# Optimization experiments

Measured on AMD Instinct MI355X. Metric: run time of the kernel, lower is better.

Reference implementation:

```python
import jax, jax.numpy as jnp
import numpy as np

N_INST = 100000
N_NET = 100000
E = 1600000
H = 64
OUT = 32
L = 2


def setup_inputs() -> dict:
    key = jax.random.key(0)
    ks = jax.random.split(key, 16)
    inp = {
        "x_inst": jax.random.normal(ks[0], (N_INST, H), jnp.float32),
        "x_net": jax.random.normal(ks[1], (N_NET, H), jnp.float32),
        "edge_i2n": jax.random.randint(ks[2], (2, E), 0, N_INST, jnp.int32),
        "edge_n2i": jax.random.randint(ks[3], (2, E), 0, N_NET, jnp.int32),
        # stacked GAT params: axis0 = layer, axis1 = relation (0: inst->net, 1: net->inst)
        "W_src": jax.random.normal(ks[4], (L, 2, H, H), jnp.float32) * 0.1,
        "W_dst": jax.random.normal(ks[5], (L, 2, H, H), jnp.float32) * 0.1,
        "att_src": jax.random.normal(ks[6], (L, 2, H), jnp.float32) * 0.1,
        "att_dst": jax.random.normal(ks[7], (L, 2, H), jnp.float32) * 0.1,
        "bias_g": jax.random.normal(ks[8], (L, 2, H), jnp.float32) * 0.1,
        "lin1_w": jax.random.normal(ks[9], (H, OUT), jnp.float32) * 0.1,
        "lin1_b": jax.random.normal(ks[10], (OUT,), jnp.float32) * 0.1,
        "lin2_w": jax.random.normal(ks[11], (OUT, 1), jnp.float32) * 0.1,
        "lin2_b": jax.random.normal(ks[12], (1,), jnp.float32) * 0.1,
    }
    return inp


def _segment_softmax(scores, seg, n_seg):
    # numerically stable softmax over edges grouped by destination node
    m = jax.ops.segment_max(scores, seg, num_segments=n_seg)
    e = jnp.exp(scores - m[seg])
    s = jax.ops.segment_sum(e, seg, num_segments=n_seg)
    return e / (s[seg] + 1e-16)


def _gat_conv(x_src, x_dst, edge, Ws, Wd, a_s, a_d, b, n_dst):
    # PyG GATConv, heads=1, add_self_loops=False, eval mode (dropout inactive)
    hs = x_src @ Ws  # [Ns, H]
    hd = x_dst @ Wd  # [Nd, H]
    src, dst = edge[0], edge[1]
    score = (hs * a_s).sum(-1)[src] + (hd * a_d).sum(-1)[dst]  # [E]
    alpha = _segment_softmax(jax.nn.leaky_relu(score, 0.2), dst, n_dst)
    out = jax.ops.segment_sum(hs[src] * alpha[:, None], dst, num_segments=n_dst)
    return out + b


def reference(x_inst, x_net, edge_i2n, edge_n2i, W_src, W_dst, att_src, att_dst,
              bias_g, lin1_w, lin1_b, lin2_w, lin2_b):
    xi, xn = x_inst, x_net
    for l in range(L):
        new_net = _gat_conv(xi, xn, edge_i2n, W_src[l, 0], W_dst[l, 0],
                            att_src[l, 0], att_dst[l, 0], bias_g[l, 0], xn.shape[0])
        new_inst = _gat_conv(xn, xi, edge_n2i, W_src[l, 1], W_dst[l, 1],
                             att_src[l, 1], att_dst[l, 1], bias_g[l, 1], xi.shape[0])
        xn = jax.nn.relu(new_net)
        xi = jax.nn.relu(new_inst)
    h = jax.nn.relu(xn @ lin1_w + lin1_b)
    return h @ lin2_w + lin2_b  # [N_net, 1]
```

## Files before the change

kernel.cpp:

```cpp
#include <hip/hip_runtime.h>
#include <hip/hip_fp16.h>

#define H 64
#define BSHIFT 9
#define BUCKET 512
#define NBMAX 256
#define CHUNK 4096

__device__ __forceinline__ int bcasti(int x, int j) {
    return __builtin_amdgcn_readlane(x, j);
}
__device__ __forceinline__ float bcastf(float x, int j) {
    return __uint_as_float((unsigned)__builtin_amdgcn_readlane((int)__float_as_uint(x), j));
}

__device__ __forceinline__ float ldf(const float* p) { return *p; }
__device__ __forceinline__ float ldf(const __half* p) { return __half2float(*p); }

__global__ void wvec3_kernel(const float* __restrict__ W_dst, const float* __restrict__ att_dst,
                             float* __restrict__ v2all) {
    int b = blockIdx.x;
    int k = threadIdx.x;
    const float* Wd = W_dst + (size_t)b * H * H;
    const float* ad = att_dst + (size_t)b * H;
    float s2 = 0.f;
    for (int j = 0; j < H; ++j) s2 += Wd[k * H + j] * ad[j];
    v2all[b * H + k] = s2;
}

template <typename T>
__device__ __forceinline__ void proj_body(float* __restrict__ Wl, int blk,
                                          const T* __restrict__ x, const float* __restrict__ W,
                                          const float* __restrict__ as_, const float* __restrict__ v2d,
                                          __half* __restrict__ hs, float* __restrict__ ssrc,
                                          float* __restrict__ sdst_out, int n) {
    int t = threadIdx.x;
    for (int i = t; i < H * H; i += 256) Wl[i] = W[i];
    __syncthreads();
    int lane = t & 63;
    int w = t >> 6;
    int row0 = blk * 16 + w * 4;
    if (row0 >= n) return;
    int rem = n - row0;
    float asl = as_[lane];
    const T* xp = x + (size_t)row0 * H + lane;
    float xr0 = ldf(xp);
    float xr1 = rem > 1 ? ldf(xp + H) : 0.f;
    float xr2 = rem > 2 ? ldf(xp + 2 * H) : 0.f;
    float xr3 = rem > 3 ? ldf(xp + 3 * H) : 0.f;
    float a0 = 0.f, a1 = 0.f, a2 = 0.f, a3 = 0.f;
#pragma unroll
    for (int k = 0; k < H; ++k) {
        float wv = Wl[k * H + lane];
        a0 = fmaf(bcastf(xr0, k), wv, a0);
        a1 = fmaf(bcastf(xr1, k), wv, a1);
        a2 = fmaf(bcastf(xr2, k), wv, a2);
        a3 = fmaf(bcastf(xr3, k), wv, a3);
    }
    __half* hp = hs + (size_t)row0 * H + lane;
    hp[0] = __float2half_rn(a0);
    if (rem > 1) hp[H] = __float2half_rn(a1);
    if (rem > 2) hp[2 * H] = __float2half_rn(a2);
    if (rem > 3) hp[3 * H] = __float2half_rn(a3);
    float p0 = a0 * asl, p1 = a1 * asl, p2 = a2 * asl, p3 = a3 * asl;
#pragma unroll
    for (int off = 32; off; off >>= 1) {
        p0 += __shfl_xor(p0, off); p1 += __shfl_xor(p1, off);
        p2 += __shfl_xor(p2, off); p3 += __shfl_xor(p3, off);
    }
    if (lane == 0) {
        ssrc[row0] = p0;
        if (rem > 1) ssrc[row0 + 1] = p1;
        if (rem > 2) ssrc[row0 + 2] = p2;
        if (rem > 3) ssrc[row0 + 3] = p3;
    }
    if (sdst_out) {
        float vl = v2d[lane];
        float q0 = xr0 * vl, q1 = xr1 * vl, q2 = xr2 * vl, q3 = xr3 * vl;
#pragma unroll
        for (int off = 32; off; off >>= 1) {
            q0 += __shfl_xor(q0, off); q1 += __shfl_xor(q1, off);
            q2 += __shfl_xor(q2, off); q3 += __shfl_xor(q3, off);
        }
        if (lane == 0) {
            sdst_out[row0] = q0;
            if (rem > 1) sdst_out[row0 + 1] = q1;
            if (rem > 2) sdst_out[row0 + 2] = q2;
            if (rem > 3) sdst_out[row0 + 3] = q3;
        }
    }
}

__global__ void hist_proj_kernel(const int* __restrict__ dstA, const int* __restrict__ dstB,
                                 int* __restrict__ cntA, int* __restrict__ cntB,
                                 int ne, int nch, int nbA, int nbB,
                                 const float* __restrict__ x, const float* __restrict__ W,
                                 const float* __restrict__ as_, const float* __restrict__ v2d,
                                 __half* __restrict__ hs, float* __restrict__ ssrc,
                                 float* __restrict__ sdst_out, int n) {
    __shared__ float smem[H * H];
    int blk = blockIdx.x;
    if (blk < 2 * nch) {
        int* h = (int*)smem;
        bool second = blk >= nch;
        const int* dst = second ? dstB : dstA;
        int* cnt = second ? cntB : cntA;
        int nb = second ? nbB : nbA;
        int c = second ? blk - nch : blk;
        int beg = c * CHUNK, end = beg + CHUNK;
        if (end > ne) end = ne;
        int t = threadIdx.x;
        for (int i = t; i < NBMAX; i += 256) h[i] = 0;
        __syncthreads();
        for (int i = beg + t; i < end; i += 256) atomicAdd(&h[dst[i] >> BSHIFT], 1);
        __syncthreads();
        for (int b = t; b < nb; b += 256) cnt[(size_t)b * nch + c] = h[b];
        return;
    }
    proj_body<float>(smem, blk - 2 * nch, x, W, as_, v2d, hs, ssrc, sdst_out, n);
}

__global__ void scan_chunks(int* __restrict__ cntA, int* __restrict__ cntB,
                            int* __restrict__ totA, int* __restrict__ totB,
                            int nch, int nbA) {
    __shared__ int sm[512];
    int b = blockIdx.x;
    bool second = b >= nbA;
    int* cnt = second ? cntB : cntA;
    int* tot = second ? totB : totA;
    if (second) b -= nbA;
    int t = threadIdx.x;
    int v = t < nch ? cnt[(size_t)b * nch + t] : 0;
    sm[t] = v;
    __syncthreads();
    for (int off = 1; off < 512; off <<= 1) {
        int u = t >= off ? sm[t - off] : 0;
        __syncthreads();
        sm[t] += u;
        __syncthreads();
    }
    if (t < nch) cnt[(size_t)b * nch + t] = sm[t] - v;
    if (t == 511) tot[b] = sm[511];
}

__global__ void scan_buckets(const int* __restrict__ totA, const int* __restrict__ totB,
                             int* __restrict__ bstartA, int* __restrict__ bstartB,
                             int nbA, int nbB, int ne) {
    __shared__ int sm[256];
    const int* tot = blockIdx.x ? totB : totA;
    int* bstart = blockIdx.x ? bstartB : bstartA;
    int nb = blockIdx.x ? nbB : nbA;
    int t = threadIdx.x;
    int v = t < nb ? tot[t] : 0;
    sm[t] = v;
    __syncthreads();
    for (int off = 1; off < 256; off <<= 1) {
        int u = t >= off ? sm[t - off] : 0;
        __syncthreads();
        sm[t] += u;
        __syncthreads();
    }
    if (t < nb) bstart[t] = sm[t] - v;
    if (t == 0) bstart[nb] = ne;
}

__global__ void scatter_proj_kernel(const int* __restrict__ srcA, const int* __restrict__ dstA,
                                    const int* __restrict__ cntA, const int* __restrict__ bstartA,
                                    unsigned* __restrict__ tmpA,
                                    const int* __restrict__ srcB, const int* __restrict__ dstB,
                                    const int* __restrict__ cntB, const int* __restrict__ bstartB,
                                    unsigned* __restrict__ tmpB,
                                    int ne, int nch, int nbA, int nbB,
                                    const float* __restrict__ x, const float* __restrict__ W,
                                    const float* __restrict__ as_, const float* __restrict__ v2d,
                                    __half* __restrict__ hs, float* __restrict__ ssrc,
                                    float* __restrict__ sdst_out, int n) {
    __shared__ float smem[H * H];
    int blk = blockIdx.x;
    if (blk < 2 * nch) {
        int* cur = (int*)smem;
        bool second = blk >= nch;
        const int* src = second ? srcB : srcA;
        const int* dst = second ? dstB : dstA;
        const int* cnt = second ? cntB : cntA;
        const int* bstart = second ? bstartB : bstartA;
        unsigned* tmp = second ? tmpB : tmpA;
        int nb = second ? nbB : nbA;
        int c = second ? blk - nch : blk;
        int beg = c * CHUNK, end = beg + CHUNK;
        if (end > ne) end = ne;
        int t = threadIdx.x;
        for (int b = t; b < nb; b += 256) cur[b] = bstart[b] + cnt[(size_t)b * nch + c];
        __syncthreads();
        for (int i = beg + t; i < end; i += 256) {
            int d = dst[i];
            int pos = atomicAdd(&cur[d >> BSHIFT], 1);
            unsigned rec = ((unsigned)(d & (BUCKET - 1)) << 17) | (unsigned)src[i];
            tmp[pos] = rec;
        }
        return;
    }
    proj_body<float>(smem, blk - 2 * nch, x, W, as_, v2d, hs, ssrc, sdst_out, n);
}

__global__ void proj_half_kernel(const __half* __restrict__ x, const float* __restrict__ W,
                                 const float* __restrict__ as_,
                                 __half* __restrict__ hs, float* __restrict__ ssrc, int n) {
    __shared__ float smem[H * H];
    proj_body<__half>(smem, blockIdx.x, x, W, as_, nullptr, hs, ssrc, nullptr, n);
}

__global__ void bucket_finalize(const unsigned* __restrict__ tmpA, const int* __restrict__ bstartA,
                                int* __restrict__ rowptrA, int* __restrict__ srcsA,
                                int ndstA, int nbA,
                                const unsigned* __restrict__ tmpB, const int* __restrict__ bstartB,
                                int* __restrict__ rowptrB, int* __restrict__ srcsB,
                                int ndstB) {
    __shared__ int cnt[BUCKET];
    __shared__ int sm[BUCKET];
    __shared__ int cur[BUCKET];
    int b = blockIdx.x;
    bool second = b >= nbA;
    const unsigned* tmp = second ? tmpB : tmpA;
    const int* bstart = second ? bstartB : bstartA;
    int* rowptr = second ? rowptrB : rowptrA;
    int* srcs   = second ? srcsB : srcsA;
    int ndst    = second ? ndstB : ndstA;
    if (second) b -= nbA;

    int t = threadIdx.x;
    int base = bstart[b], endi = bstart[b + 1];
    cnt[t] = 0;
    __syncthreads();
    for (int i = base + t; i < endi; i += 512)
        atomicAdd(&cnt[tmp[i] >> 17], 1);
    __syncthreads();
    int c0 = cnt[t];
    sm[t] = c0;
    __syncthreads();
    for (int off = 1; off < 512; off <<= 1) {
        int u = t >= off ? sm[t - off] : 0;
        __syncthreads();
        sm[t] += u;
        __syncthreads();
    }
    int d0 = b << BSHIFT;
    int e = base + sm[t] - c0;
    cur[t] = e;
    if (d0 + t < ndst) rowptr[d0 + t] = e;
    if (t == 0) {
        int hi = d0 + BUCKET;
        if (hi > ndst) hi = ndst;
        rowptr[hi] = endi;
    }
    __syncthreads();
    for (int i = base + t; i < endi; i += 512) {
        unsigned rec = tmp[i];
        int pos = atomicAdd(&cur[rec >> 17], 1);
        srcs[pos] = (int)(rec & 0x1FFFFu);
    }
}

template <int P>
__device__ __forceinline__ float gat_fast(const int* __restrict__ srcs, int beg, int cnt,
                                          const float* __restrict__ ssrc, float sdst,
                                          const __half* __restrict__ hs,
                                          const float* __restrict__ bias, int lane) {
    bool valid = lane < cnt;
    int s_l = valid ? srcs[beg + lane] : 0;
    float ss = valid ? ssrc[s_l] : 0.f;

    const __half* hsl = hs + lane;
    __half hv[P];
#pragma unroll
    for (int k = 0; k < P; ++k) {
        hv[k] = hsl[(size_t)bcasti(s_l, k) * H];
    }

    float sc = ss + sdst;
    sc = sc > 0.f ? sc : 0.2f * sc;
    float ev_l = valid ? __expf(sc) : 0.f;
    float ll = ev_l;
#pragma unroll
    for (int off = 32; off; off >>= 1) ll += __shfl_xor(ll, off);

    float acc0 = 0.f, acc1 = 0.f, acc2 = 0.f, acc3 = 0.f;
    float acc4 = 0.f, acc5 = 0.f, acc6 = 0.f, acc7 = 0.f;
#pragma unroll
    for (int k = 0; k < P; k += 8) {
        acc0 += bcastf(ev_l, k + 0) * __half2float(hv[k + 0]);
        acc1 += bcastf(ev_l, k + 1) * __half2float(hv[k + 1]);
        acc2 += bcastf(ev_l, k + 2) * __half2float(hv[k + 2]);
        acc3 += bcastf(ev_l, k + 3) * __half2float(hv[k + 3]);
        acc4 += bcastf(ev_l, k + 4) * __half2float(hv[k + 4]);
        acc5 += bcastf(ev_l, k + 5) * __half2float(hv[k + 5]);
        acc6 += bcastf(ev_l, k + 6) * __half2float(hv[k + 6]);
        acc7 += bcastf(ev_l, k + 7) * __half2float(hv[k + 7]);
    }
    if constexpr (P == 32) {
        int j = P;
        for (; j + 3 < cnt; j += 4) {
            acc0 += bcastf(ev_l, j + 0) * __half2float(hsl[(size_t)bcasti(s_l, j + 0) * H]);
            acc1 += bcastf(ev_l, j + 1) * __half2float(hsl[(size_t)bcasti(s_l, j + 1) * H]);
            acc2 += bcastf(ev_l, j + 2) * __half2float(hsl[(size_t)bcasti(s_l, j + 2) * H]);
            acc3 += bcastf(ev_l, j + 3) * __half2float(hsl[(size_t)bcasti(s_l, j + 3) * H]);
        }
        for (; j < cnt; ++j)
            acc0 += bcastf(ev_l, j) * __half2float(hsl[(size_t)bcasti(s_l, j) * H]);
    }
    float v = ((acc0 + acc1) + (acc2 + acc3)) + ((acc4 + acc5) + (acc6 + acc7));
    v = v / (ll + 1e-16f) + bias[lane];
    return v > 0.f ? v : 0.f;
}

__device__ __forceinline__ float gat_general(const int* __restrict__ srcs, int beg, int end,
                                             const float* __restrict__ ssrc, float sdst,
                                             const __half* __restrict__ hs,
                                             const float* __restrict__ bias, int lane) {
    const __half* hsl = hs + lane;
    float acc0 = 0.f, acc1 = 0.f;
    float mm = -3.4e38f;
    for (int base = beg; base < end; base += 64) {
        int idx = base + lane;
        if (idx < end) {
            float sc = ssrc[srcs[idx]] + sdst;
            sc = sc > 0.f ? sc : 0.2f * sc;
            mm = fmaxf(mm, sc);
        }
    }
#pragma unroll
    for (int off = 32; off; off >>= 1) mm = fmaxf(mm, __shfl_xor(mm, off));
    float ll = 0.f;
    for (int base = beg; base < end; base += 64) {
        int idx = base + lane;
        int c2 = end - base; if (c2 > 64) c2 = 64;
        int s_l = idx < end ? srcs[idx] : 0;
        float ev_l = 0.f;
        if (idx < end) {
            float sc = ssrc[s_l] + sdst;
            sc = sc > 0.f ? sc : 0.2f * sc;
            ev_l = __expf(sc - mm);
        }
        ll += ev_l;
        int j = 0;
        for (; j + 1 < c2; j += 2) {
            acc0 += bcastf(ev_l, j) * __half2float(hsl[(size_t)bcasti(s_l, j) * H]);
            acc1 += bcastf(ev_l, j + 1) * __half2float(hsl[(size_t)bcasti(s_l, j + 1) * H]);
        }
        if (j < c2)
            acc0 += bcastf(ev_l, j) * __half2float(hsl[(size_t)bcasti(s_l, j) * H]);
    }
#pragma unroll
    for (int off = 32; off; off >>= 1) ll += __shfl_xor(ll, off);
    float v = (acc0 + acc1) / (ll + 1e-16f) + bias[lane];
    return v > 0.f ? v : 0.f;
}

__device__ __forceinline__ float gat_aggregate(const int* __restrict__ rowptr,
                                               const int* __restrict__ srcs,
                                               const float* __restrict__ ssrc,
                                               float sdst,
                                               const __half* __restrict__ hs,
                                               const float* __restrict__ bias,
                                               int wid, int lane) {
    int beg = rowptr[wid], end = rowptr[wid + 1];
    int cnt = end - beg;
    if (cnt <= 16) return gat_fast<16>(srcs, beg, cnt, ssrc, sdst, hs, bias, lane);
    if (cnt <= 64) return gat_fast<32>(srcs, beg, cnt, ssrc, sdst, hs, bias, lane);
    return gat_general(srcs, beg, end, ssrc, sdst, hs, bias, lane);
}

template <int P>
__device__ __forceinline__ float2 gat_pair_fast(const int* __restrict__ srcs,
                                                int r0, int r1, int cnt0, int cnt1,
                                                const float* __restrict__ ssrc,
                                                float sdstA, float sdstB,
                                                const __half* __restrict__ hs,
                                                const float* __restrict__ bias,
                                                int lane) {
    int half = lane >> 5, sub = lane & 31;
    int beg = half ? r1 : r0;
    int cnt = half ? cnt1 : cnt0;
    bool valid = sub < cnt;
    int s_l = valid ? srcs[beg + sub] : 0;
    float ss = valid ? ssrc[s_l] : 0.f;
    float sdst = half ? sdstB : sdstA;

    const __half2* hp = (const __half2*)hs;
    __half2 hv[P];
#pragma unroll
    for (int k = 0; k < P; ++k) {
        int sA = bcasti(s_l, k), sB = bcasti(s_l, 32 + k);
        int srow = half ? sB : sA;
        hv[k] = hp[(size_t)srow * 32 + sub];
    }

    float sc = ss + sdst;
    sc = sc > 0.f ? sc : 0.2f * sc;
    float ev_l = valid ? __expf(sc) : 0.f;
    float ll = ev_l;
#pragma unroll
    for (int off = 16; off; off >>= 1) ll += __shfl_xor(ll, off);

    float ax0 = 0.f, ax1 = 0.f, ax2 = 0.f, ax3 = 0.f;
    float ay0 = 0.f, ay1 = 0.f, ay2 = 0.f, ay3 = 0.f;
#pragma unroll
    for (int k = 0; k < P; k += 4) {
#pragma unroll
        for (int u = 0; u < 4; ++u) {
            float eA = bcastf(ev_l, k + u), eB = bcastf(ev_l, 32 + k + u);
            float e = half ? eB : eA;
            float2 f = __half22float2(hv[k + u]);
            if (u == 0) { ax0 += e * f.x; ay0 += e * f.y; }
            if (u == 1) { ax1 += e * f.x; ay1 += e * f.y; }
            if (u == 2) { ax2 += e * f.x; ay2 += e * f.y; }
            if (u == 3) { ax3 += e * f.x; ay3 += e * f.y; }
        }
    }
    float vx = (ax0 + ax1) + (ax2 + ax3);
    float vy = (ay0 + ay1) + (ay2 + ay3);
    float inv = 1.f / (ll + 1e-16f);
    float2 bv = *(const float2*)(bias + 2 * sub);
    vx = vx * inv + bv.x;
    vy = vy * inv + bv.y;
    vx = vx > 0.f ? vx : 0.f;
    vy = vy > 0.f ? vy : 0.f;
    return make_float2(vx, vy);
}

__global__ void gat1_kernel(const int* __restrict__ rp, const int* __restrict__ sr,
                            const float* __restrict__ ssrc, const float* __restrict__ sdstArr,
                            const __half* __restrict__ hs, const float* __restrict__ bias,
                            __half* __restrict__ out, int n) {
    int t = (int)(blockIdx.x * blockDim.x + threadIdx.x);
    int pw = t >> 6, lane = t & 63;
    int wid0 = 2 * pw;
    if (wid0 >= n) return;
    bool has1 = wid0 + 1 < n;
    int r0 = rp[wid0], r1 = rp[wid0 + 1];
    int r2 = has1 ? rp[wid0 + 2] : r1;
    int cnt0 = r1 - r0, cnt1 = r2 - r1;
    int mx = cnt0 > cnt1 ? cnt0 : cnt1;
    int half = lane >> 5, sub = lane & 31;

    if (mx <= 32) {
        float sdstA = sdstArr[wid0];
        float sdstB = has1 ? sdstArr[wid0 + 1] : 0.f;
        float2 v;
        if (mx <= 16) v = gat_pair_fast<16>(sr, r0, r1, cnt0, cnt1, ssrc, sdstA, sdstB, hs, bias, lane);
        else          v = gat_pair_fast<32>(sr, r0, r1, cnt0, cnt1, ssrc, sdstA, sdstB, hs, bias, lane);
        int node = half ? wid0 + 1 : wid0;
        if (!half || has1)
            *(__half2*)(out + (size_t)node * H + 2 * sub) = __float22half2_rn(v);
    } else {
        float v0 = gat_aggregate(rp, sr, ssrc, sdstArr[wid0], hs, bias, wid0, lane);
        out[(size_t)wid0 * H + lane] = __float2half_rn(v0);
        if (has1) {
            float v1 = gat_aggregate(rp, sr, ssrc, sdstArr[wid0 + 1], hs, bias, wid0 + 1, lane);
            out[(size_t)(wid0 + 1) * H + lane] = __float2half_rn(v1);
        }
    }
}

template <int P>
__device__ __forceinline__ float gat02_fast(const int* __restrict__ srcs, int beg, int cnt,
                                            const float* __restrict__ ssrc0, float sdst0,
                                            const __half* __restrict__ hs0, const float* __restrict__ bias0,
                                            const float* __restrict__ v2next,
                                            const float* __restrict__ ssrc2,
                                            const __half* __restrict__ hs2, const float* __restrict__ bias2,
                                            int lane) {
    bool valid = lane < cnt;
    int s_l = valid ? srcs[beg + lane] : 0;
    float ss0 = valid ? ssrc0[s_l] : 0.f;
    float ss2 = valid ? ssrc2[s_l] : 0.f;

    const __half* h0 = hs0 + lane;
    const __half* h2 = hs2 + lane;
    __half hv0[P], hv2[P];
#pragma unroll
    for (int k = 0; k < P; ++k) hv0[k] = h0[(size_t)bcasti(s_l, k) * H];
#pragma unroll
    for (int k = 0; k < P; ++k) hv2[k] = h2[(size_t)bcasti(s_l, k) * H];

    float sc0 = ss0 + sdst0;
    sc0 = sc0 > 0.f ? sc0 : 0.2f * sc0;
    float ev0 = valid ? __expf(sc0) : 0.f;
    float l0 = ev0;
#pragma unroll
    for (int off = 32; off; off >>= 1) l0 += __shfl_xor(l0, off);

    float a0 = 0.f, a1 = 0.f, a2 = 0.f, a3 = 0.f;
#pragma unroll
    for (int k = 0; k < P; k += 4) {
        a0 += bcastf(ev0, k + 0) * __half2float(hv0[k + 0]);
        a1 += bcastf(ev0, k + 1) * __half2float(hv0[k + 1]);
        a2 += bcastf(ev0, k + 2) * __half2float(hv0[k + 2]);
        a3 += bcastf(ev0, k + 3) * __half2float(hv0[k + 3]);
    }
    if constexpr (P == 32) {
        int j = P;
        for (; j < cnt; ++j)
            a0 += bcastf(ev0, j) * __half2float(h0[(size_t)bcasti(s_l, j) * H]);
    }
    float v0 = ((a0 + a1) + (a2 + a3)) / (l0 + 1e-16f) + bias0[lane];
    v0 = v0 > 0.f ? v0 : 0.f;

    float q = v0 * v2next[lane];
#pragma unroll
    for (int off = 32; off; off >>= 1) q += __shfl_xor(q, off);

    float sc2 = ss2 + q;
    sc2 = sc2 > 0.f ? sc2 : 0.2f * sc2;
    float ev2 = valid ? __expf(sc2) : 0.f;
    float l2 = ev2;
#pragma unroll
    for (int off = 32; off; off >>= 1) l2 += __shfl_xor(l2, off);

    float b0 = 0.f, b1 = 0.f, b2_ = 0.f, b3 = 0.f;
#pragma unroll
    for (int k = 0; k < P; k += 4) {
        b0 += bcastf(ev2, k + 0) * __half2float(hv2[k + 0]);
        b1 += bcastf(ev2, k + 1) * __half2float(hv2[k + 1]);
        b2_ += bcastf(ev2, k + 2) * __half2float(hv2[k + 2]);
        b3 += bcastf(ev2, k + 3) * __half2float(hv2[k + 3]);
    }
    if constexpr (P == 32) {
        int j = P;
        for (; j < cnt; ++j)
            b0 += bcastf(ev2, j) * __half2float(h2[(size_t)bcasti(s_l, j) * H]);
    }
    float v2 = ((b0 + b1) + (b2_ + b3)) / (l2 + 1e-16f) + bias2[lane];
    return v2 > 0.f ? v2 : 0.f;
}

__global__ void gat02_mlp_kernel(const int* __restrict__ rowptr, const int* __restrict__ srcs,
                                 const float* __restrict__ ssrc0, const float* __restrict__ sdst0Arr,
                                 const __half* __restrict__ hs0, const float* __restrict__ bias0,
                                 const float* __restrict__ v2next,
                                 const float* __restrict__ ssrc2, const __half* __restrict__ hs2,
                                 const float* __restrict__ bias2,
                                 const float* __restrict__ w1, const float* __restrict__ b1,
                                 const float* __restrict__ w2, const float* __restrict__ b2,
                                 float* __restrict__ out, int ndst) {
    __shared__ float W1[H * 32];
    __shared__ float W2[32];
    __shared__ float B1[32];
    {
        int t = threadIdx.x;
        for (int i = t; i < H * 32; i += 256) W1[i] = w1[i];
        if (t < 32) { W2[t] = w2[t]; B1[t] = b1[t]; }
        __syncthreads();
    }
    int wid = (int)((blockIdx.x * blockDim.x + threadIdx.x) >> 6);
    int lane = threadIdx.x & 63;
    if (wid >= ndst) return;

    int beg = rowptr[wid], end = rowptr[wid + 1];
    int cnt = end - beg;
    float v;
    if (cnt <= 16) {
        v = gat02_fast<16>(srcs, beg, cnt, ssrc0, sdst0Arr[wid], hs0, bias0,
                           v2next, ssrc2, hs2, bias2, lane);
    } else if (cnt <= 64) {
        v = gat02_fast<32>(srcs, beg, cnt, ssrc0, sdst0Arr[wid], hs0, bias0,
                           v2next, ssrc2, hs2, bias2, lane);
    } else {
        float v0 = gat_general(srcs, beg, end, ssrc0, sdst0Arr[wid], hs0, bias0, lane);
        float q = v0 * v2next[lane];
#pragma unroll
        for (int off = 32; off; off >>= 1) q += __shfl_xor(q, off);
        v = gat_general(srcs, beg, end, ssrc2, q, hs2, bias2, lane);
    }

    int c = lane & 31;
    int kbase = (lane >> 5) << 5;
    float s = 0.f;
#pragma unroll
    for (int k = 0; k < 32; ++k) s += __shfl(v, kbase + k) * W1[(kbase + k) * 32 + c];
    s += __shfl_xor(s, 32);
    s += B1[c];
    s = s > 0.f ? s : 0.f;
    float q = s * W2[c];
#pragma unroll
    for (int off = 16; off; off >>= 1) q += __shfl_xor(q, off);
    if (lane == 0) out[wid] = q + b2[0];
}

extern "C" void kernel_launch(void* const* d_in, const int* in_sizes, int n_in,
                              void* d_out, int out_size, void* d_ws, size_t ws_size,
                              hipStream_t stream) {
    const float* x_inst  = (const float*)d_in[0];
    const float* x_net   = (const float*)d_in[1];
    const int*   e_i2n   = (const int*)d_in[2];
    const int*   e_n2i   = (const int*)d_in[3];
    const float* W_src   = (const float*)d_in[4];
    const float* W_dst   = (const float*)d_in[5];
    const float* att_src = (const float*)d_in[6];
    const float* att_dst = (const float*)d_in[7];
    const float* bias_g  = (const float*)d_in[8];
    const float* lin1_w  = (const float*)d_in[9];
    const float* lin1_b  = (const float*)d_in[10];
    const float* lin2_w  = (const float*)d_in[11];
    const float* lin2_b  = (const float*)d_in[12];

    const int n_inst = in_sizes[0] / H;
    const int n_net  = in_sizes[1] / H;
    const int ne     = in_sizes[2] / 2;
    const int nmax   = n_inst > n_net ? n_inst : n_net;

    const int nbA = (n_net + BUCKET - 1) >> BSHIFT;
    const int nbB = (n_inst + BUCKET - 1) >> BSHIFT;
    const int nch = (ne + CHUNK - 1) / CHUNK;

    float* ws = (float*)d_ws;
    size_t off = 0;
    auto alloc = [&](size_t nelem) {
        off = (off + 3) & ~(size_t)3;
        float* p = ws + off; off += nelem; return p;
    };
    __half* xiA    = (__half*)alloc((size_t)n_inst * H / 2);
    __half* hs0    = (__half*)alloc((size_t)nmax * H / 2);
    __half* hs1    = (__half*)alloc((size_t)nmax * H / 2);
    __half* hs2    = (__half*)alloc((size_t)nmax * H / 2);
    float* ssrc0   = alloc(nmax);
    float* ssrc1   = alloc(nmax);
    float* ssrc2   = alloc(nmax);
    float* sdstA   = alloc(nmax);
    float* sdstB   = alloc(nmax);
    int*   rp_i2n  = (int*)alloc(nmax + 1);
    int*   sr_i2n  = (int*)alloc(ne);
    int*   rp_n2i  = (int*)alloc(nmax + 1);
    int*   sr_n2i  = (int*)alloc(ne);
    unsigned* tmpA = (unsigned*)alloc(ne);
    unsigned* tmpB = (unsigned*)alloc(ne);
    int*   cntA    = (int*)alloc((size_t)NBMAX * nch);
    int*   cntB    = (int*)alloc((size_t)NBMAX * nch);
    int*   totA    = (int*)alloc(NBMAX);
    int*   totB    = (int*)alloc(NBMAX);
    int*   bstartA = (int*)alloc(NBMAX + 1);
    int*   bstartB = (int*)alloc(NBMAX + 1);
    float* v2all   = alloc(3 * H);
    (void)ws_size;

    const int* dstA = e_i2n + ne;
    const int* dstB = e_n2i + ne;

    wvec3_kernel<<<3, 64, 0, stream>>>(W_dst, att_dst, v2all);

    {
        int grid = 2 * nch + (n_inst + 15) / 16;
        hist_proj_kernel<<<grid, 256, 0, stream>>>(dstA, dstB, cntA, cntB, ne, nch, nbA, nbB,
                                                   x_inst, W_src + 0 * H * H, att_src + 0 * H,
                                                   v2all + 1 * H, hs0, ssrc0, sdstB, n_inst);
    }
    scan_chunks<<<nbA + nbB, 512, 0, stream>>>(cntA, cntB, totA, totB, nch, nbA);
    scan_buckets<<<2, 256, 0, stream>>>(totA, totB, bstartA, bstartB, nbA, nbB, ne);
    {
        int grid = 2 * nch + (n_net + 15) / 16;
        scatter_proj_kernel<<<grid, 256, 0, stream>>>(e_i2n, dstA, cntA, bstartA, tmpA,
                                                      e_n2i, dstB, cntB, bstartB, tmpB,
                                                      ne, nch, nbA, nbB,
                                                      x_net, W_src + 1 * H * H, att_src + 1 * H,
                                                      v2all + 0 * H, hs1, ssrc1, sdstA, n_net);
    }
    bucket_finalize<<<nbA + nbB, 512, 0, stream>>>(tmpA, bstartA, rp_i2n, sr_i2n, n_net, nbA,
                                                   tmpB, bstartB, rp_n2i, sr_n2i, n_inst);

    {
        int npair = (n_inst + 1) / 2;
        gat1_kernel<<<(npair + 3) / 4, 256, 0, stream>>>(rp_n2i, sr_n2i, ssrc1, sdstB,
                                                         hs1, bias_g + 1 * H, xiA, n_inst);
    }
    proj_half_kernel<<<(n_inst + 15) / 16, 256, 0, stream>>>(xiA, W_src + 2 * H * H,
                                                             att_src + 2 * H, hs2, ssrc2, n_inst);
    gat02_mlp_kernel<<<(n_net + 3) / 4, 256, 0, stream>>>(rp_i2n, sr_i2n,
                                                          ssrc0, sdstA, hs0, bias_g + 0 * H,
                                                          v2all + 2 * H,
                                                          ssrc2, hs2, bias_g + 2 * H,
                                                          lin1_w, lin1_b, lin2_w, lin2_b,
                                                          (float*)d_out, n_net);
}
```

Baseline: 330.2 us.

## Interleave layer-0 and layer-2 source features into one half2 array for gathers

The layer-0 and layer-2 projected source features (hs0, hs2) and their attention scores (ssrc0, ssrc2) are stored interleaved per row and channel, so the fused gat02 kernel fetches both with one half2 and one float2 gather per edge. This halves the number of random gather transactions in the final fused kernel. The projection kernels now write with a stride of two, so their stores are no longer contiguous and each row spans twice as many cache lines.

Measured after the change: 306.3 us. 1.08x faster.

```diff
diff --git a/kernel.cpp b/kernel.cpp
--- a/kernel.cpp
+++ b/kernel.cpp
@@ -32,7 +32,8 @@
 __device__ __forceinline__ void proj_body(float* __restrict__ Wl, int blk,
                                           const T* __restrict__ x, const float* __restrict__ W,
                                           const float* __restrict__ as_, const float* __restrict__ v2d,
-                                          __half* __restrict__ hs, float* __restrict__ ssrc,
+                                          __half* __restrict__ hs, int rstride, int cstride,
+                                          float* __restrict__ ssrc, int sstride,
                                           float* __restrict__ sdst_out, int n) {
     int t = threadIdx.x;
     for (int i = t; i < H * H; i += 256) Wl[i] = W[i];
@@ -57,11 +58,11 @@
         a2 = fmaf(bcastf(xr2, k), wv, a2);
         a3 = fmaf(bcastf(xr3, k), wv, a3);
     }
-    __half* hp = hs + (size_t)row0 * H + lane;
+    __half* hp = hs + (size_t)row0 * rstride + lane * cstride;
     hp[0] = __float2half_rn(a0);
-    if (rem > 1) hp[H] = __float2half_rn(a1);
-    if (rem > 2) hp[2 * H] = __float2half_rn(a2);
-    if (rem > 3) hp[3 * H] = __float2half_rn(a3);
+    if (rem > 1) hp[rstride] = __float2half_rn(a1);
+    if (rem > 2) hp[2 * rstride] = __float2half_rn(a2);
+    if (rem > 3) hp[3 * rstride] = __float2half_rn(a3);
     float p0 = a0 * asl, p1 = a1 * asl, p2 = a2 * asl, p3 = a3 * asl;
 #pragma unroll
     for (int off = 32; off; off >>= 1) {
@@ -69,10 +70,10 @@
         p2 += __shfl_xor(p2, off); p3 += __shfl_xor(p3, off);
     }
     if (lane == 0) {
-        ssrc[row0] = p0;
-        if (rem > 1) ssrc[row0 + 1] = p1;
-        if (rem > 2) ssrc[row0 + 2] = p2;
-        if (rem > 3) ssrc[row0 + 3] = p3;
+        ssrc[(size_t)row0 * sstride] = p0;
+        if (rem > 1) ssrc[(size_t)(row0 + 1) * sstride] = p1;
+        if (rem > 2) ssrc[(size_t)(row0 + 2) * sstride] = p2;
+        if (rem > 3) ssrc[(size_t)(row0 + 3) * sstride] = p3;
     }
     if (sdst_out) {
         float vl = v2d[lane];
@@ -96,7 +97,7 @@
                                  int ne, int nch, int nbA, int nbB,
                                  const float* __restrict__ x, const float* __restrict__ W,
                                  const float* __restrict__ as_, const float* __restrict__ v2d,
-                                 __half* __restrict__ hs, float* __restrict__ ssrc,
+                                 __half* __restrict__ hs02, float* __restrict__ ssrc02,
                                  float* __restrict__ sdst_out, int n) {
     __shared__ float smem[H * H];
     int blk = blockIdx.x;
@@ -117,7 +118,8 @@
         for (int b = t; b < nb; b += 256) cnt[(size_t)b * nch + c] = h[b];
         return;
     }
-    proj_body<float>(smem, blk - 2 * nch, x, W, as_, v2d, hs, ssrc, sdst_out, n);
+    proj_body<float>(smem, blk - 2 * nch, x, W, as_, v2d,
+                     hs02, 2 * H, 2, ssrc02, 2, sdst_out, n);
 }
 
 __global__ void scan_chunks(int* __restrict__ cntA, int* __restrict__ cntB,
@@ -200,14 +202,16 @@
         }
         return;
     }
-    proj_body<float>(smem, blk - 2 * nch, x, W, as_, v2d, hs, ssrc, sdst_out, n);
+    proj_body<float>(smem, blk - 2 * nch, x, W, as_, v2d,
+                     hs, H, 1, ssrc, 1, sdst_out, n);
 }
 
 __global__ void proj_half_kernel(const __half* __restrict__ x, const float* __restrict__ W,
                                  const float* __restrict__ as_,
-                                 __half* __restrict__ hs, float* __restrict__ ssrc, int n) {
+                                 __half* __restrict__ hs02, float* __restrict__ ssrc02, int n) {
     __shared__ float smem[H * H];
-    proj_body<__half>(smem, blockIdx.x, x, W, as_, nullptr, hs, ssrc, nullptr, n);
+    proj_body<__half>(smem, blockIdx.x, x, W, as_, nullptr,
+                      hs02 + 1, 2 * H, 2, ssrc02 + 1, 2, nullptr, n);
 }
 
 __global__ void bucket_finalize(const unsigned* __restrict__ tmpA, const int* __restrict__ bstartA,
@@ -314,16 +318,16 @@
 }
 
 __device__ __forceinline__ float gat_general(const int* __restrict__ srcs, int beg, int end,
-                                             const float* __restrict__ ssrc, float sdst,
-                                             const __half* __restrict__ hs,
+                                             const float* __restrict__ ssrc, int sstride, float sdst,
+                                             const __half* __restrict__ hs, int rstride, int cstride,
                                              const float* __restrict__ bias, int lane) {
-    const __half* hsl = hs + lane;
+    const __half* hsl = hs + lane * cstride;
     float acc0 = 0.f, acc1 = 0.f;
     float mm = -3.4e38f;
     for (int base = beg; base < end; base += 64) {
         int idx = base + lane;
         if (idx < end) {
-            float sc = ssrc[srcs[idx]] + sdst;
+            float sc = ssrc[(size_t)srcs[idx] * sstride] + sdst;
             sc = sc > 0.f ? sc : 0.2f * sc;
             mm = fmaxf(mm, sc);
         }
@@ -337,18 +341,18 @@
         int s_l = idx < end ? srcs[idx] : 0;
         float ev_l = 0.f;
         if (idx < end) {
-            float sc = ssrc[s_l] + sdst;
+            float sc = ssrc[(size_t)s_l * sstride] + sdst;
             sc = sc > 0.f ? sc : 0.2f * sc;
             ev_l = __expf(sc - mm);
         }
         ll += ev_l;
         int j = 0;
         for (; j + 1 < c2; j += 2) {
-            acc0 += bcastf(ev_l, j) * __half2float(hsl[(size_t)bcasti(s_l, j) * H]);
-            acc1 += bcastf(ev_l, j + 1) * __half2float(hsl[(size_t)bcasti(s_l, j + 1) * H]);
+            acc0 += bcastf(ev_l, j) * __half2float(hsl[(size_t)bcasti(s_l, j) * rstride]);
+            acc1 += bcastf(ev_l, j + 1) * __half2float(hsl[(size_t)bcasti(s_l, j + 1) * rstride]);
         }
         if (j < c2)
-            acc0 += bcastf(ev_l, j) * __half2float(hsl[(size_t)bcasti(s_l, j) * H]);
+            acc0 += bcastf(ev_l, j) * __half2float(hsl[(size_t)bcasti(s_l, j) * rstride]);
     }
 #pragma unroll
     for (int off = 32; off; off >>= 1) ll += __shfl_xor(ll, off);
@@ -367,7 +371,7 @@
     int cnt = end - beg;
     if (cnt <= 16) return gat_fast<16>(srcs, beg, cnt, ssrc, sdst, hs, bias, lane);
     if (cnt <= 64) return gat_fast<32>(srcs, beg, cnt, ssrc, sdst, hs, bias, lane);
-    return gat_general(srcs, beg, end, ssrc, sdst, hs, bias, lane);
+    return gat_general(srcs, beg, end, ssrc, 1, sdst, hs, H, 1, bias, lane);
 }
 
 template <int P>
@@ -464,26 +468,23 @@
 
 template <int P>
 __device__ __forceinline__ float gat02_fast(const int* __restrict__ srcs, int beg, int cnt,
-                                            const float* __restrict__ ssrc0, float sdst0,
-                                            const __half* __restrict__ hs0, const float* __restrict__ bias0,
+                                            const float* __restrict__ ssrc02, float sdst0,
+                                            const __half* __restrict__ hs02,
+                                            const float* __restrict__ bias0,
                                             const float* __restrict__ v2next,
-                                            const float* __restrict__ ssrc2,
-                                            const __half* __restrict__ hs2, const float* __restrict__ bias2,
+                                            const float* __restrict__ bias2,
                                             int lane) {
     bool valid = lane < cnt;
     int s_l = valid ? srcs[beg + lane] : 0;
-    float ss0 = valid ? ssrc0[s_l] : 0.f;
-    float ss2 = valid ? ssrc2[s_l] : 0.f;
-
-    const __half* h0 = hs0 + lane;
-    const __half* h2 = hs2 + lane;
-    __half hv0[P], hv2[P];
-#pragma unroll
-    for (int k = 0; k < P; ++k) hv0[k] = h0[(size_t)bcasti(s_l, k) * H];
-#pragma unroll
-    for (int k = 0; k < P; ++k) hv2[k] = h2[(size_t)bcasti(s_l, k) * H];
-
-    float sc0 = ss0 + sdst0;
+    float2 sspair = make_float2(0.f, 0.f);
+    if (valid) sspair = *(const float2*)(ssrc02 + 2 * (size_t)s_l);
+
+    const __half2* hrow = (const __half2*)hs02 + lane;
+    __half2 hv[P];
+#pragma unroll
+    for (int k = 0; k < P; ++k) hv[k] = hrow[(size_t)bcasti(s_l, k) * H];
+
+    float sc0 = sspair.x + sdst0;
     sc0 = sc0 > 0.f ? sc0 : 0.2f * sc0;
     float ev0 = valid ? __expf(sc0) : 0.f;
     float l0 = ev0;
@@ -493,15 +494,14 @@
     float a0 = 0.f, a1 = 0.f, a2 = 0.f, a3 = 0.f;
 #pragma unroll
     for (int k = 0; k < P; k += 4) {
-        a0 += bcastf(ev0, k + 0) * __half2float(hv0[k + 0]);
-        a1 += bcastf(ev0, k + 1) * __half2float(hv0[k + 1]);
-        a2 += bcastf(ev0, k + 2) * __half2float(hv0[k + 2]);
-        a3 += bcastf(ev0, k + 3) * __half2float(hv0[k + 3]);
+        a0 += bcastf(ev0, k + 0) * __half2float(__low2half(hv[k + 0]));
+        a1 += bcastf(ev0, k + 1) * __half2float(__low2half(hv[k + 1]));
+        a2 += bcastf(ev0, k + 2) * __half2float(__low2half(hv[k + 2]));
+        a3 += bcastf(ev0, k + 3) * __half2float(__low2half(hv[k + 3]));
     }
     if constexpr (P == 32) {
-        int j = P;
-        for (; j < cnt; ++j)
-            a0 += bcastf(ev0, j) * __half2float(h0[(size_t)bcasti(s_l, j) * H]);
+        for (int j = P; j < cnt; ++j)
+            a0 += bcastf(ev0, j) * __half2float(__low2half(hrow[(size_t)bcasti(s_l, j) * H]));
     }
     float v0 = ((a0 + a1) + (a2 + a3)) / (l0 + 1e-16f) + bias0[lane];
     v0 = v0 > 0.f ? v0 : 0.f;
@@ -510,7 +510,7 @@
 #pragma unroll
     for (int off = 32; off; off >>= 1) q += __shfl_xor(q, off);
 
-    float sc2 = ss2 + q;
+    float sc2 = sspair.y + q;
     sc2 = sc2 > 0.f ? sc2 : 0.2f * sc2;
     float ev2 = valid ? __expf(sc2) : 0.f;
     float l2 = ev2;
@@ -520,26 +520,23 @@
     float b0 = 0.f, b1 = 0.f, b2_ = 0.f, b3 = 0.f;
 #pragma unroll
     for (int k = 0; k < P; k += 4) {
-        b0 += bcastf(ev2, k + 0) * __half2float(hv2[k + 0]);
-        b1 += bcastf(ev2, k + 1) * __half2float(hv2[k + 1]);
-        b2_ += bcastf(ev2, k + 2) * __half2float(hv2[k + 2]);
-        b3 += bcastf(ev2, k + 3) * __half2float(hv2[k + 3]);
+        b0 += bcastf(ev2, k + 0) * __half2float(__high2half(hv[k + 0]));
+        b1 += bcastf(ev2, k + 1) * __half2float(__high2half(hv[k + 1]));
+        b2_ += bcastf(ev2, k + 2) * __half2float(__high2half(hv[k + 2]));
+        b3 += bcastf(ev2, k + 3) * __half2float(__high2half(hv[k + 3]));
     }
     if constexpr (P == 32) {
-        int j = P;
-        for (; j < cnt; ++j)
-            b0 += bcastf(ev2, j) * __half2float(h2[(size_t)bcasti(s_l, j) * H]);
+        for (int j = P; j < cnt; ++j)
+            b0 += bcastf(ev2, j) * __half2float(__high2half(hrow[(size_t)bcasti(s_l, j) * H]));
     }
     float v2 = ((b0 + b1) + (b2_ + b3)) / (l2 + 1e-16f) + bias2[lane];
     return v2 > 0.f ? v2 : 0.f;
 }
 
 __global__ void gat02_mlp_kernel(const int* __restrict__ rowptr, const int* __restrict__ srcs,
-                                 const float* __restrict__ ssrc0, const float* __restrict__ sdst0Arr,
-                                 const __half* __restrict__ hs0, const float* __restrict__ bias0,
-                                 const float* __restrict__ v2next,
-                                 const float* __restrict__ ssrc2, const __half* __restrict__ hs2,
-                                 const float* __restrict__ bias2,
+                                 const float* __restrict__ ssrc02, const float* __restrict__ sdst0Arr,
+                                 const __half* __restrict__ hs02, const float* __restrict__ bias0,
+                                 const float* __restrict__ v2next, const float* __restrict__ bias2,
                                  const float* __restrict__ w1, const float* __restrict__ b1,
                                  const float* __restrict__ w2, const float* __restrict__ b2,
                                  float* __restrict__ out, int ndst) {
@@ -560,17 +557,15 @@
     int cnt = end - beg;
     float v;
     if (cnt <= 16) {
-        v = gat02_fast<16>(srcs, beg, cnt, ssrc0, sdst0Arr[wid], hs0, bias0,
-                           v2next, ssrc2, hs2, bias2, lane);
+        v = gat02_fast<16>(srcs, beg, cnt, ssrc02, sdst0Arr[wid], hs02, bias0, v2next, bias2, lane);
     } else if (cnt <= 64) {
-        v = gat02_fast<32>(srcs, beg, cnt, ssrc0, sdst0Arr[wid], hs0, bias0,
-                           v2next, ssrc2, hs2, bias2, lane);
+        v = gat02_fast<32>(srcs, beg, cnt, ssrc02, sdst0Arr[wid], hs02, bias0, v2next, bias2, lane);
     } else {
-        float v0 = gat_general(srcs, beg, end, ssrc0, sdst0Arr[wid], hs0, bias0, lane);
+        float v0 = gat_general(srcs, beg, end, ssrc02, 2, sdst0Arr[wid], hs02, 2 * H, 2, bias0, lane);
         float q = v0 * v2next[lane];
 #pragma unroll
         for (int off = 32; off; off >>= 1) q += __shfl_xor(q, off);
-        v = gat_general(srcs, beg, end, ssrc2, q, hs2, bias2, lane);
+        v = gat_general(srcs, beg, end, ssrc02 + 1, 2, q, hs02 + 1, 2 * H, 2, bias2, lane);
     }
 
     int c = lane & 31;
@@ -620,12 +615,10 @@
         float* p = ws + off; off += nelem; return p;
     };
     __half* xiA    = (__half*)alloc((size_t)n_inst * H / 2);
-    __half* hs0    = (__half*)alloc((size_t)nmax * H / 2);
+    __half* hs02   = (__half*)alloc((size_t)nmax * H);
     __half* hs1    = (__half*)alloc((size_t)nmax * H / 2);
-    __half* hs2    = (__half*)alloc((size_t)nmax * H / 2);
-    float* ssrc0   = alloc(nmax);
+    float* ssrc02  = alloc((size_t)nmax * 2);
     float* ssrc1   = alloc(nmax);
-    float* ssrc2   = alloc(nmax);
     float* sdstA   = alloc(nmax);
     float* sdstB   = alloc(nmax);
     int*   rp_i2n  = (int*)alloc(nmax + 1);
@@ -652,7 +645,7 @@
         int grid = 2 * nch + (n_inst + 15) / 16;
         hist_proj_kernel<<<grid, 256, 0, stream>>>(dstA, dstB, cntA, cntB, ne, nch, nbA, nbB,
                                                    x_inst, W_src + 0 * H * H, att_src + 0 * H,
-                                                   v2all + 1 * H, hs0, ssrc0, sdstB, n_inst);
+                                                   v2all + 1 * H, hs02, ssrc02, sdstB, n_inst);
     }
     scan_chunks<<<nbA + nbB, 512, 0, stream>>>(cntA, cntB, totA, totB, nch, nbA);
     scan_buckets<<<2, 256, 0, stream>>>(totA, totB, bstartA, bstartB, nbA, nbB, ne);
@@ -673,11 +666,10 @@
                                                          hs1, bias_g + 1 * H, xiA, n_inst);
     }
     proj_half_kernel<<<(n_inst + 15) / 16, 256, 0, stream>>>(xiA, W_src + 2 * H * H,
-                                                             att_src + 2 * H, hs2, ssrc2, n_inst);
+                                                             att_src + 2 * H, hs02, ssrc02, n_inst);
     gat02_mlp_kernel<<<(n_net + 3) / 4, 256, 0, stream>>>(rp_i2n, sr_i2n,
-                                                          ssrc0, sdstA, hs0, bias_g + 0 * H,
-                                                          v2all + 2 * H,
-                                                          ssrc2, hs2, bias_g + 2 * H,
+                                                          ssrc02, sdstA, hs02, bias_g + 0 * H,
+                                                          v2all + 2 * H, bias_g + 2 * H,
                                                           lin1_w, lin1_b, lin2_w, lin2_b,
                                                           (float*)d_out, n_net);
 }
```
